# Kernel tuning notes

Measured on AMD Instinct MI355X. Metric: run time of the kernel, lower is better.

Reference implementation:

```python
import jax, jax.numpy as jnp
import numpy as np

B, S, H, V = 32, 512, 768, 30522
N_UPDATE, MAX_LEN = 3, 8
NEG_INF = -1e9


def setup_inputs() -> dict:
    key = jax.random.key(0)
    ks = jax.random.split(key, 12)
    x = jax.random.randint(ks[0], (B, S), 0, V, dtype=jnp.int32)
    decoder_input = jax.random.normal(ks[1], (B, N_UPDATE, H), dtype=jnp.float32)
    encoder_output = jax.random.normal(ks[2], (B, S, H), dtype=jnp.float32)
    hidden = jax.random.normal(ks[3], (1, B, H), dtype=jnp.float32)
    teacher = jax.random.randint(ks[4], (B, N_UPDATE, MAX_LEN), 0, V, dtype=jnp.int32)
    # tied embedding table, padding_idx=0 row zeroed
    embed_w = (jax.random.normal(ks[5], (V, H), dtype=jnp.float32) * 0.02).at[0].set(0.0)
    # GRU weights ~ N(0, initializer_range=0.02), biases zero (torch default biases exist; keep small random)
    gru_w_ih = jax.random.normal(ks[6], (3 * H, H), dtype=jnp.float32) * 0.02
    gru_w_hh = jax.random.normal(ks[7], (3 * H, H), dtype=jnp.float32) * 0.02
    gru_b_ih = jax.random.normal(ks[8], (3 * H,), dtype=jnp.float32) * 0.02
    gru_b_hh = jax.random.normal(ks[9], (3 * H,), dtype=jnp.float32) * 0.02
    wgen_w = jax.random.normal(ks[10], (1, 3 * H), dtype=jnp.float32) * 0.02
    wgen_b = jnp.zeros((1,), dtype=jnp.float32)
    return {"x": x, "decoder_input": decoder_input, "encoder_output": encoder_output,
            "hidden": hidden, "teacher": teacher, "embed_w": embed_w,
            "gru_w_ih": gru_w_ih, "gru_w_hh": gru_w_hh, "gru_b_ih": gru_b_ih,
            "gru_b_hh": gru_b_hh, "wgen_w": wgen_w, "wgen_b": wgen_b, "max_len": MAX_LEN}


def _gru_cell(w, h, w_ih, w_hh, b_ih, b_hh):
    # PyTorch GRU cell. w, h: [B, H]
    gi = w @ w_ih.T + b_ih  # [B, 3H]
    gh = h @ w_hh.T + b_hh
    i_r, i_z, i_n = jnp.split(gi, 3, axis=-1)
    h_r, h_z, h_n = jnp.split(gh, 3, axis=-1)
    r = jax.nn.sigmoid(i_r + h_r)
    z = jax.nn.sigmoid(i_z + h_z)
    n = jnp.tanh(i_n + r * h_n)
    return (1.0 - z) * n + z * h


def reference(x, decoder_input, encoder_output, hidden, teacher, embed_w,
              gru_w_ih, gru_w_hh, gru_b_ih, gru_b_hh, wgen_w, wgen_b, max_len):
    b, n_update, hid = decoder_input.shape
    vocab = embed_w.shape[0]
    mask = (x == 0)  # [B, S]
    bidx = jnp.arange(b)[:, None]

    # Teacher-forced inputs: step 0 of slot j uses decoder_input[:, j];
    # step k>0 uses embed(teacher[:, j, k-1]).
    teacher_emb = embed_w[teacher]                     # [B, nU, L, H]
    inputs = jnp.concatenate([decoder_input[:, :, None, :], teacher_emb[:, :, :-1, :]], axis=2)
    inputs = inputs.transpose(1, 2, 0, 3).reshape(n_update * max_len, b, hid)  # [nU*L, B, H]

    h0 = hidden[0]  # [B, H]

    def step(h, w):
        h = _gru_cell(w, h, gru_w_ih, gru_w_hh, gru_b_ih, gru_b_hh)
        attn_e = jnp.einsum('bsh,bh->bs', encoder_output, h)
        attn_e = jnp.where(mask, NEG_INF, attn_e)
        attn_history = jax.nn.softmax(attn_e, axis=-1)          # [B, S]
        attn_vocab = jax.nn.softmax(h @ embed_w.T, axis=-1)     # [B, V]
        context = jnp.einsum('bs,bsh->bh', attn_history, encoder_output)
        p_gen = jax.nn.sigmoid(jnp.concatenate([w, h, context], axis=-1) @ wgen_w.T + wgen_b)  # [B,1]
        p_ctx = jnp.zeros((b, vocab), dtype=attn_vocab.dtype).at[bidx, x].add(attn_history)
        p_final = p_gen * attn_vocab + (1.0 - p_gen) * p_ctx    # [B, V]
        return h, p_final

    _, p_all = jax.lax.scan(step, h0, inputs)                    # [nU*L, B, V]
    p_all = p_all.reshape(n_update, max_len, b, vocab).transpose(2, 0, 1, 3)
    return p_all  # [B, n_update, max_len, V]
```

## Files before the change

### kernel.cpp

```cpp
#include <hip/hip_runtime.h>
#include <cstdint>

#define B_  32
#define S_  512
#define H_  768
#define V_  30522
#define NT_ 24
#define H3  2304
#define NC4   (V_*H_/4)
#define NWALL (NT_*B_*H_)
#define NINIT (B_*H_)

#define GRU_NBLK 192
#define GRU_TPB  512
#define GRU_JPB  4
#define GRU_RPB  12

typedef unsigned short ushort_t;
typedef __attribute__((ext_vector_type(8))) short bf16x8;
typedef __attribute__((ext_vector_type(4))) float f32x4;

__device__ __forceinline__ ushort_t f2bf(float f){
  union { float f; unsigned u; } v; v.f = f;
  unsigned r = v.u + 0x7fffu + ((v.u >> 16) & 1u);
  return (ushort_t)(r >> 16);
}

__device__ __forceinline__ void load_lds_16B(const void* g, void* l){
  auto gp = reinterpret_cast<const __attribute__((address_space(1))) unsigned int*>(
      reinterpret_cast<uintptr_t>(g));
  auto lp = reinterpret_cast<__attribute__((address_space(3))) unsigned int*>(
      reinterpret_cast<uintptr_t>(l));
  __builtin_amdgcn_global_load_lds(gp, lp, 16, 0, 0);
}

__global__ void k_prep(const float* __restrict__ embed, const float* __restrict__ dec,
                       const int* __restrict__ teacher, const float* __restrict__ hidden,
                       ushort_t* __restrict__ E2, float* __restrict__ wall,
                       float* __restrict__ wallT, float* __restrict__ Hq, float* __restrict__ Hb,
                       float* __restrict__ pgacc, unsigned* __restrict__ flags){
  int idx = blockIdx.x * 256 + threadIdx.x;
  if (idx < NC4){
    float4 v = ((const float4*)embed)[idx];
    uint2 o;
    o.x = (unsigned)f2bf(v.x) | ((unsigned)f2bf(v.y) << 16);
    o.y = (unsigned)f2bf(v.z) | ((unsigned)f2bf(v.w) << 16);
    ((uint2*)E2)[idx] = o;
    return;
  }
  idx -= NC4;
  if (idx < NWALL){
    int k  = idx % H_;
    int rb = idx / H_;
    int t = rb >> 5, b = rb & 31;
    int jj = t >> 3, kk = t & 7;
    float v;
    if (kk == 0) v = dec[(b*3 + jj)*H_ + k];
    else { int tok = teacher[(b*3 + jj)*8 + kk - 1]; v = embed[(size_t)tok*H_ + k]; }
    wall[idx] = v;
    wallT[(size_t)t*24576 + ((k >> 1)*B_ + b)*2 + (k & 1)] = v;
    return;
  }
  idx -= NWALL;
  if (idx < NINIT){
    int b = idx / H_, k = idx % H_;
    float v = hidden[idx];
    Hb[idx] = v;
    Hq[((k >> 1)*B_ + b)*2 + (k & 1)] = v;
    return;
  }
  idx -= NINIT;
  if (idx < 768){ pgacc[idx] = 0.f; return; }
  idx -= 768;
  if (idx < 768) flags[idx] = 0u;
}

__global__ __launch_bounds__(GRU_TPB) void k_gru_all(const float* __restrict__ wallT, const float* __restrict__ wih,
                                                     const float* __restrict__ whh, const float* __restrict__ bih,
                                                     const float* __restrict__ bhh, const float* __restrict__ hidden,
                                                     float* __restrict__ Hq, float* __restrict__ Hb,
                                                     ushort_t* __restrict__ A2, unsigned* __restrict__ flags){
  __shared__ float wsh[GRU_RPB*768];
  __shared__ float wsi[GRU_RPB*768];
  __shared__ float red[16*776];
  __shared__ float bsh[GRU_RPB], bsi[GRU_RPB];
  const int tid = threadIdx.x;
  const int j0 = blockIdx.x * GRU_JPB;

  for (int idx4 = tid; idx4 < GRU_RPB*192; idx4 += GRU_TPB){
    int r = idx4 / 192, k4 = idx4 % 192;
    int gate = r >> 2, jl = r & 3;
    *(float4*)&wsh[r*768 + k4*4] = *(const float4*)&whh[(size_t)(gate*768 + j0 + jl)*768 + k4*4];
    *(float4*)&wsi[r*768 + k4*4] = *(const float4*)&wih[(size_t)(gate*768 + j0 + jl)*768 + k4*4];
  }
  if (tid < GRU_RPB){
    bsh[tid] = bhh[(tid >> 2)*768 + j0 + (tid & 3)];
    bsi[tid] = bih[(tid >> 2)*768 + j0 + (tid & 3)];
  }
  __syncthreads();

  const int ks = tid >> 5, b = tid & 31;
  const int jl = tid >> 5, bb = tid & 31;
  const int j  = j0 + (jl & 3);
  float hp = 0.f;
  if (tid < 128) hp = hidden[bb*768 + j];

  for (int t = 0; t < NT_; ++t){
    const unsigned long long* hsrc = (const unsigned long long*)(Hq + (size_t)t*24576);
    const float2* wsrc = (const float2*)(wallT + (size_t)t*24576);

    float acch[GRU_RPB], acci[GRU_RPB];
#pragma unroll
    for (int r = 0; r < GRU_RPB; ++r){ acch[r] = 0.f; acci[r] = 0.f; }
#pragma unroll 4
    for (int i = 0; i < 24; ++i){
      union { unsigned long long u; float f[2]; } cv;
      cv.u = __hip_atomic_load(&hsrc[(size_t)(ks*24 + i)*32 + b],
                               __ATOMIC_RELAXED, __HIP_MEMORY_SCOPE_AGENT);
      const float2 wv = wsrc[(size_t)(ks*24 + i)*32 + b];
      const float h0 = cv.f[0], h1 = cv.f[1];
#pragma unroll
      for (int r = 0; r < GRU_RPB; ++r){
        const float2 wh = *(const float2*)&wsh[r*768 + ks*48 + i*2];
        const float2 wi = *(const float2*)&wsi[r*768 + ks*48 + i*2];
        acch[r] += h0*wh.x + h1*wh.y;
        acci[r] += wv.x*wi.x + wv.y*wi.y;
      }
    }
#pragma unroll
    for (int r = 0; r < GRU_RPB; ++r){
      red[ks*776 + r*32 + b]             = acch[r];
      red[ks*776 + (GRU_RPB + r)*32 + b] = acci[r];
    }
    __syncthreads();

    if (tid < 128){
      float aR = 0.f, aZ = 0.f, aN = 0.f, iR = 0.f, iZ = 0.f, iN = 0.f;
#pragma unroll
      for (int k8 = 0; k8 < 16; ++k8){
        const float* rb_ = &red[k8*776 + jl*32 + bb];
        aR += rb_[0*128]; aZ += rb_[1*128]; aN += rb_[2*128];
        iR += rb_[3*128]; iZ += rb_[4*128]; iN += rb_[5*128];
      }
      aR += bsh[jl]; aZ += bsh[4 + jl]; aN += bsh[8 + jl];
      const float ir = iR + bsi[jl], iz = iZ + bsi[4 + jl], inn = iN + bsi[8 + jl];
      float rg = 1.f / (1.f + __expf(-(ir + aR)));
      float zg = 1.f / (1.f + __expf(-(iz + aZ)));
      float e2 = __expf(-2.f*(inn + rg * aN));
      float ng = (1.f - e2) / (1.f + e2);
      float hn = (1.f - zg)*ng + zg*hp;
      hp = hn;
      Hb[(size_t)(t+1)*24576 + bb*768 + j] = hn;
      A2[(size_t)(t*32 + bb)*768 + j] = f2bf(hn);
      if (t < NT_ - 1){
        union { float f; unsigned u; } hv; hv.f = hn;
        unsigned* hq32 = (unsigned*)(Hq + (size_t)(t+1)*24576);
        __hip_atomic_store(&hq32[((j >> 1)*32 + bb)*2 + (j & 1)], hv.u,
                           __ATOMIC_RELAXED, __HIP_MEMORY_SCOPE_AGENT);
      }
    }
    __syncthreads();

    if (t < NT_ - 1){
      if (tid == 0)
        __hip_atomic_store(&flags[(size_t)blockIdx.x*4], (unsigned)(t + 1),
                           __ATOMIC_RELAXED, __HIP_MEMORY_SCOPE_AGENT);
      if (tid < GRU_NBLK){
        unsigned spins = 0u;
        while (__hip_atomic_load(&flags[(size_t)tid*4], __ATOMIC_RELAXED,
                                 __HIP_MEMORY_SCOPE_AGENT) < (unsigned)(t + 1) &&
               ++spins < 20000000u)
          __builtin_amdgcn_s_sleep(1);
      }
      __syncthreads();
    }
  }
}

__global__ __launch_bounds__(256) void k_attn(const float* __restrict__ enc, const float* __restrict__ Hb1,
                                              float* __restrict__ ae){
  __shared__ float Es[64*36];
  __shared__ float Ht[24*36];
  const int b = blockIdx.x, s0 = blockIdx.y * 64;
  const int tid = threadIdx.x;
  const int s_l = tid & 63, tq = tid >> 6;
  const int r = tid >> 2, kq = tid & 3;
  float acc[6] = {0.f,0.f,0.f,0.f,0.f,0.f};
  for (int k0 = 0; k0 < 768; k0 += 32){
    __syncthreads();
    float4 e0 = *(const float4*)&enc[(size_t)(b*512 + s0 + r)*768 + k0 + kq*8];
    float4 e1 = *(const float4*)&enc[(size_t)(b*512 + s0 + r)*768 + k0 + kq*8 + 4];
    *(float4*)&Es[r*36 + kq*8]     = e0;
    *(float4*)&Es[r*36 + kq*8 + 4] = e1;
    if (tid < 192){
      int t = tid >> 3, k4 = tid & 7;
      *(float4*)&Ht[t*36 + k4*4] = *(const float4*)&Hb1[(size_t)t*24576 + b*768 + k0 + k4*4];
    }
    __syncthreads();
#pragma unroll
    for (int k4 = 0; k4 < 8; ++k4){
      float4 e = *(const float4*)&Es[s_l*36 + k4*4];
#pragma unroll
      for (int i = 0; i < 6; ++i){
        float4 h4 = *(const float4*)&Ht[(tq*6 + i)*36 + k4*4];
        acc[i] += e.x*h4.x + e.y*h4.y + e.z*h4.z + e.w*h4.w;
      }
    }
  }
#pragma unroll
  for (int i = 0; i < 6; ++i)
    ae[(size_t)((tq*6 + i)*32 + b)*512 + s0 + s_l] = acc[i];
}

__global__ __launch_bounds__(256) void k_attnsoft(const int* __restrict__ x, float* __restrict__ ae){
  const int row = blockIdx.x;
  const int b = row & 31;
  const int tid = threadIdx.x;
  __shared__ float red[256];
  float v0 = ae[(size_t)row*512 + tid];
  float v1 = ae[(size_t)row*512 + 256 + tid];
  if (x[b*512 + tid]        == 0) v0 = -1e9f;
  if (x[b*512 + 256 + tid]  == 0) v1 = -1e9f;
  float m = fmaxf(v0, v1);
  red[tid] = m; __syncthreads();
  for (int off = 128; off; off >>= 1){ if (tid < off) red[tid] = fmaxf(red[tid], red[tid+off]); __syncthreads(); }
  float M = red[0]; __syncthreads();
  float e0 = __expf(v0 - M), e1 = __expf(v1 - M);
  red[tid] = e0 + e1; __syncthreads();
  for (int off = 128; off; off >>= 1){ if (tid < off) red[tid] += red[tid+off]; __syncthreads(); }
  float inv = 1.f / red[0];
  ae[(size_t)row*512 + tid]       = e0 * inv;
  ae[(size_t)row*512 + 256 + tid] = e1 * inv;
}

__global__ __launch_bounds__(256) void k_ctx_pgen(const float* __restrict__ enc, const float* __restrict__ ah,
                                                  const float* __restrict__ wall, const float* __restrict__ Hb1,
                                                  const float* __restrict__ wg, float* __restrict__ pgacc){
  const int b = blockIdx.x;
  const int klane = threadIdx.x & 63;
  const int k = blockIdx.y * 64 + klane;
  const int tq = threadIdx.x >> 6;
  float acc[6] = {0.f,0.f,0.f,0.f,0.f,0.f};
  for (int s4 = 0; s4 < 512; s4 += 4){
    float e0 = enc[(size_t)(b*512 + s4 + 0)*768 + k];
    float e1 = enc[(size_t)(b*512 + s4 + 1)*768 + k];
    float e2 = enc[(size_t)(b*512 + s4 + 2)*768 + k];
    float e3 = enc[(size_t)(b*512 + s4 + 3)*768 + k];
#pragma unroll
    for (int i = 0; i < 6; ++i){
      float4 a4 = *(const float4*)&ah[(size_t)((tq*6 + i)*32 + b)*512 + s4];
      acc[i] = fmaf(a4.x, e0, acc[i]); acc[i] = fmaf(a4.y, e1, acc[i]);
      acc[i] = fmaf(a4.z, e2, acc[i]); acc[i] = fmaf(a4.w, e3, acc[i]);
    }
  }
  const float wgk = wg[k], wgh = wg[768 + k], wgc = wg[1536 + k];
#pragma unroll
  for (int i = 0; i < 6; ++i){
    const int t = tq*6 + i, row = t*32 + b;
    float p = acc[i]*wgc + wall[(size_t)row*768 + k]*wgk + Hb1[(size_t)t*24576 + b*768 + k]*wgh;
#pragma unroll
    for (int off = 32; off; off >>= 1) p += __shfl_down(p, off, 64);
    if (klane == 0) atomicAdd(&pgacc[row], p);
  }
}

__global__ __launch_bounds__(256) void k_vgemm(const ushort_t* __restrict__ A2, const ushort_t* __restrict__ E2,
                                               float* __restrict__ out){
  __shared__ ushort_t ldsA[128*64];
  __shared__ ushort_t ldsB[128*64];
  const int wg = blockIdx.x;
  const int xcd = wg & 7, qq = wg >> 3;
  const int ntile = (qq / 6) * 8 + xcd;
  const int mtile = qq % 6;
  const int tid = threadIdx.x;
  const int w = tid >> 6, lane = tid & 63;
  const int lrow = lane >> 3, lpos = lane & 7;
  const int wm = w >> 1, wn = w & 1;
  const int q = lane >> 4, fr = lane & 15;
  f32x4 acc[4][4];
  f32x4 zero = {0.f, 0.f, 0.f, 0.f};
#pragma unroll
  for (int a = 0; a < 4; ++a)
#pragma unroll
    for (int c = 0; c < 4; ++c) acc[a][c] = zero;

  for (int k0 = 0; k0 < 768; k0 += 64){
    __syncthreads();
#pragma unroll
    for (int i = 0; i < 4; ++i){
      int row = w*32 + i*8 + lrow;
      int c   = lpos ^ (row & 7);
      const ushort_t* srcA = A2 + (size_t)(mtile*128 + row)*768 + k0 + c*8;
      int brow = ntile*128 + row; if (brow > V_ - 1) brow = V_ - 1;
      const ushort_t* srcB = E2 + (size_t)brow*768 + k0 + c*8;
      load_lds_16B(srcA, &ldsA[row*64 + lpos*8]);
      load_lds_16B(srcB, &ldsB[row*64 + lpos*8]);
    }
    __builtin_amdgcn_s_waitcnt(0);
    __syncthreads();
#pragma unroll
    for (int s = 0; s < 2; ++s){
      bf16x8 af[4], bfr[4];
#pragma unroll
      for (int mt = 0; mt < 4; ++mt){
        int row = wm*64 + mt*16 + fr;
        int ch = (s*4 + q) ^ (row & 7);
        af[mt] = *(const bf16x8*)&ldsA[row*64 + ch*8];
      }
#pragma unroll
      for (int nt = 0; nt < 4; ++nt){
        int row = wn*64 + nt*16 + fr;
        int ch = (s*4 + q) ^ (row & 7);
        bfr[nt] = *(const bf16x8*)&ldsB[row*64 + ch*8];
      }
#pragma unroll
      for (int mt = 0; mt < 4; ++mt)
#pragma unroll
        for (int nt = 0; nt < 4; ++nt)
          acc[mt][nt] = __builtin_amdgcn_mfma_f32_16x16x32_bf16(af[mt], bfr[nt], acc[mt][nt], 0, 0, 0);
    }
  }
#pragma unroll
  for (int mt = 0; mt < 4; ++mt){
#pragma unroll
    for (int nt = 0; nt < 4; ++nt){
      int gn = ntile*128 + wn*64 + nt*16 + fr;
      if (gn >= V_) continue;
#pragma unroll
      for (int rg = 0; rg < 4; ++rg){
        int gm = mtile*128 + wm*64 + mt*16 + q*4 + rg;
        int t = gm >> 5, b = gm & 31;
        out[(size_t)(b*24 + t)*V_ + gn] = acc[mt][nt][rg];
      }
    }
  }
}

__global__ __launch_bounds__(512) void k_vsoft(float* __restrict__ out, const float* __restrict__ pgacc,
                                               const float* __restrict__ wgb){
  const int row = blockIdx.x;
  const int b = row / 24, t = row % 24;
  const float pg = 1.f / (1.f + __expf(-(pgacc[t*32 + b] + wgb[0])));
  const int tid = threadIdx.x;
  float* rp = out + (size_t)row * V_;
  const float4* rp4 = (const float4*)rp;
  float m = -3.0e38f, s = 0.f;
  for (int i = tid; i < 7630; i += 512){
    float4 v = rp4[i];
    float vm = fmaxf(fmaxf(v.x, v.y), fmaxf(v.z, v.w));
    float vs = __expf(v.x - vm) + __expf(v.y - vm) + __expf(v.z - vm) + __expf(v.w - vm);
    float nm = fmaxf(m, vm);
    s = s * __expf(m - nm) + vs * __expf(vm - nm);
    m = nm;
  }
  if (tid < 2){
    float v = rp[30520 + tid];
    float nm = fmaxf(m, v);
    s = s * __expf(m - nm) + __expf(v - nm);
    m = nm;
  }
#pragma unroll
  for (int off = 1; off < 64; off <<= 1){
    float m2 = __shfl_xor(m, off, 64), s2 = __shfl_xor(s, off, 64);
    float nm = fmaxf(m, m2);
    s = s*__expf(m - nm) + s2*__expf(m2 - nm);
    m = nm;
  }
  __shared__ float rm[8], rs[8];
  const int wid = tid >> 6;
  if ((tid & 63) == 0){ rm[wid] = m; rs[wid] = s; }
  __syncthreads();
  if (tid == 0){
    float M = rm[0], S = rs[0];
#pragma unroll
    for (int i = 1; i < 8; ++i){
      float m2 = rm[i], s2 = rs[i];
      float nm = fmaxf(M, m2);
      S = S*__expf(M - nm) + s2*__expf(m2 - nm);
      M = nm;
    }
    rm[0] = M; rs[0] = pg / S;
  }
  __syncthreads();
  const float M = rm[0], inv = rs[0];
  for (int i = tid; i < 7630; i += 512){
    float4 v = rp4[i];
    v.x = __expf(v.x - M) * inv;
    v.y = __expf(v.y - M) * inv;
    v.z = __expf(v.z - M) * inv;
    v.w = __expf(v.w - M) * inv;
    ((float4*)rp)[i] = v;
  }
  if (tid < 2) rp[30520 + tid] = __expf(rp[30520 + tid] - M) * inv;
}

__global__ void k_scatter(const float* __restrict__ ah, const float* __restrict__ pgacc,
                          const float* __restrict__ wgb, const int* __restrict__ x,
                          float* __restrict__ out){
  int idx = blockIdx.x * 256 + threadIdx.x;
  int s = idx & 511;
  int row = idx >> 9;
  int t = row >> 5, b = row & 31;
  float pg = 1.f / (1.f + __expf(-(pgacc[row] + wgb[0])));
  float val = ah[idx] * (1.f - pg);
  int col = x[b*512 + s];
  atomicAdd(&out[(size_t)(b*24 + t)*V_ + col], val);
}

extern "C" void kernel_launch(void* const* d_in, const int* in_sizes, int n_in,
                              void* d_out, int out_size, void* d_ws, size_t ws_size,
                              hipStream_t stream){
  (void)in_sizes; (void)n_in; (void)out_size; (void)ws_size;
  const int*   x      = (const int*)  d_in[0];
  const float* dec    = (const float*)d_in[1];
  const float* enc    = (const float*)d_in[2];
  const float* hidden = (const float*)d_in[3];
  const int*   teach  = (const int*)  d_in[4];
  const float* embed  = (const float*)d_in[5];
  const float* wih    = (const float*)d_in[6];
  const float* whh    = (const float*)d_in[7];
  const float* bih    = (const float*)d_in[8];
  const float* bhh    = (const float*)d_in[9];
  const float* wg     = (const float*)d_in[10];
  const float* wgb    = (const float*)d_in[11];
  float* out = (float*)d_out;

  char* p = (char*)d_ws;
  auto alloc = [&](size_t bytes){ void* r = (void*)p; p += (bytes + 255) & ~(size_t)255; return r; };
  ushort_t* E2  = (ushort_t*)alloc((size_t)V_ * H_ * 2);
  ushort_t* A2  = (ushort_t*)alloc((size_t)768 * 768 * 2);
  float* wall   = (float*)alloc((size_t)NT_ * B_ * H_ * 4);
  float* wallT  = (float*)alloc((size_t)NT_ * B_ * H_ * 4);
  float* Hb     = (float*)alloc((size_t)(NT_+1) * B_ * H_ * 4);
  float* Hq     = (float*)alloc((size_t)(NT_+1) * B_ * H_ * 4);
  float* ae     = (float*)alloc((size_t)NT_ * B_ * S_ * 4);
  float* pgacc  = (float*)alloc(768 * 4);
  unsigned* flags = (unsigned*)alloc(768 * 4);

  const int prep_items  = NC4 + NWALL + NINIT + 768 + 768;
  const int prep_blocks = (prep_items + 255) / 256;

  k_prep<<<prep_blocks, 256, 0, stream>>>(embed, dec, teach, hidden, E2, wall, wallT, Hq, Hb, pgacc, flags);
  k_gru_all<<<GRU_NBLK, GRU_TPB, 0, stream>>>(wallT, wih, whh, bih, bhh, hidden, Hq, Hb, A2, flags);
  k_attn<<<dim3(32, 8), 256, 0, stream>>>(enc, Hb + 24576, ae);
  k_attnsoft<<<768, 256, 0, stream>>>(x, ae);
  k_ctx_pgen<<<dim3(32, 12), 256, 0, stream>>>(enc, ae, wall, Hb + 24576, wg, pgacc);
  k_vgemm<<<1440, 256, 0, stream>>>(A2, E2, out);
  k_vsoft<<<768, 512, 0, stream>>>(out, pgacc, wgb);
  k_scatter<<<(NT_*B_*S_)/256, 256, 0, stream>>>(ae, pgacc, wgb, x, out);
}
```

Before: 706.4 us.

## Fuse softmax partial stats into vocab GEMM epilogue and scatter into softmax

The vocab GEMM epilogue now computes per-tile online max/sum-exp for each output row and writes them to a small stats buffer. The softmax kernel merges these tile stats instead of re-reading each 30522-wide row for the max/sum pass. The scatter-add of attention is folded into the end of the softmax kernel, with block-local atomics removing one launch. The GRU inner loop is also reworked to batch its global loads into registers and use float4 LDS reads, at the cost of more registers.

```diff
diff --git a/kernel.cpp b/kernel.cpp
--- a/kernel.cpp
+++ b/kernel.cpp
@@ -15,6 +15,7 @@
 #define GRU_TPB  512
 #define GRU_JPB  4
 #define GRU_RPB  12
+#define NTILE_   240
 
 typedef unsigned short ushort_t;
 typedef __attribute__((ext_vector_type(8))) short bf16x8;
@@ -112,19 +113,33 @@
     float acch[GRU_RPB], acci[GRU_RPB];
 #pragma unroll
     for (int r = 0; r < GRU_RPB; ++r){ acch[r] = 0.f; acci[r] = 0.f; }
-#pragma unroll 4
-    for (int i = 0; i < 24; ++i){
-      union { unsigned long long u; float f[2]; } cv;
-      cv.u = __hip_atomic_load(&hsrc[(size_t)(ks*24 + i)*32 + b],
-                               __ATOMIC_RELAXED, __HIP_MEMORY_SCOPE_AGENT);
-      const float2 wv = wsrc[(size_t)(ks*24 + i)*32 + b];
-      const float h0 = cv.f[0], h1 = cv.f[1];
-#pragma unroll
-      for (int r = 0; r < GRU_RPB; ++r){
-        const float2 wh = *(const float2*)&wsh[r*768 + ks*48 + i*2];
-        const float2 wi = *(const float2*)&wsi[r*768 + ks*48 + i*2];
-        acch[r] += h0*wh.x + h1*wh.y;
-        acci[r] += wv.x*wi.x + wv.y*wi.y;
+
+#pragma unroll
+    for (int c = 0; c < 2; ++c){
+      unsigned long long hreg[12];
+      float2 wreg[12];
+#pragma unroll
+      for (int i = 0; i < 12; ++i)
+        hreg[i] = __hip_atomic_load(&hsrc[(size_t)(ks*24 + c*12 + i)*32 + b],
+                                    __ATOMIC_RELAXED, __HIP_MEMORY_SCOPE_AGENT);
+#pragma unroll
+      for (int i = 0; i < 12; ++i)
+        wreg[i] = wsrc[(size_t)(ks*24 + c*12 + i)*32 + b];
+
+#pragma unroll
+      for (int p = 0; p < 6; ++p){
+        union { unsigned long long u; float f[2]; } ca, cb;
+        ca.u = hreg[2*p]; cb.u = hreg[2*p + 1];
+        const float h0a = ca.f[0], h1a = ca.f[1], h0b = cb.f[0], h1b = cb.f[1];
+        const float2 wa = wreg[2*p], wb = wreg[2*p + 1];
+        const int wo = ks*48 + c*24 + p*4;
+#pragma unroll
+        for (int r = 0; r < GRU_RPB; ++r){
+          const float4 wh = *(const float4*)&wsh[r*768 + wo];
+          const float4 wi = *(const float4*)&wsi[r*768 + wo];
+          acch[r] += h0a*wh.x + h1a*wh.y + h0b*wh.z + h1b*wh.w;
+          acci[r] += wa.x*wi.x + wa.y*wi.y + wb.x*wi.z + wb.y*wi.w;
+        }
       }
     }
 #pragma unroll
@@ -265,9 +280,10 @@
 }
 
 __global__ __launch_bounds__(256) void k_vgemm(const ushort_t* __restrict__ A2, const ushort_t* __restrict__ E2,
-                                               float* __restrict__ out){
+                                               float* __restrict__ out, float2* __restrict__ vstat){
   __shared__ ushort_t ldsA[128*64];
   __shared__ ushort_t ldsB[128*64];
+  __shared__ float smx[128*2], sms[128*2];
   const int wg = blockIdx.x;
   const int xcd = wg & 7, qq = wg >> 3;
   const int ntile = (qq / 6) * 8 + xcd;
@@ -323,41 +339,57 @@
 #pragma unroll
   for (int mt = 0; mt < 4; ++mt){
 #pragma unroll
-    for (int nt = 0; nt < 4; ++nt){
-      int gn = ntile*128 + wn*64 + nt*16 + fr;
-      if (gn >= V_) continue;
-#pragma unroll
-      for (int rg = 0; rg < 4; ++rg){
-        int gm = mtile*128 + wm*64 + mt*16 + q*4 + rg;
-        int t = gm >> 5, b = gm & 31;
-        out[(size_t)(b*24 + t)*V_ + gn] = acc[mt][nt][rg];
-      }
-    }
-  }
-}
-
-__global__ __launch_bounds__(512) void k_vsoft(float* __restrict__ out, const float* __restrict__ pgacc,
-                                               const float* __restrict__ wgb){
+    for (int rg = 0; rg < 4; ++rg){
+      float m = -3.0e38f, ssum = 0.f;
+#pragma unroll
+      for (int nt = 0; nt < 4; ++nt){
+        int gn = ntile*128 + wn*64 + nt*16 + fr;
+        if (gn < V_){
+          float v = acc[mt][nt][rg];
+          int gm = mtile*128 + wm*64 + mt*16 + q*4 + rg;
+          int t = gm >> 5, b = gm & 31;
+          out[(size_t)(b*24 + t)*V_ + gn] = v;
+          float nm = fmaxf(m, v);
+          ssum = ssum*__expf(m - nm) + __expf(v - nm);
+          m = nm;
+        }
+      }
+#pragma unroll
+      for (int off = 1; off < 16; off <<= 1){
+        float m2 = __shfl_xor(m, off, 64), s2 = __shfl_xor(ssum, off, 64);
+        float nm = fmaxf(m, m2);
+        ssum = ssum*__expf(m - nm) + s2*__expf(m2 - nm);
+        m = nm;
+      }
+      if (fr == 0){
+        int rl = wm*64 + mt*16 + q*4 + rg;
+        smx[rl*2 + wn] = m; sms[rl*2 + wn] = ssum;
+      }
+    }
+  }
+  __syncthreads();
+  if (tid < 128){
+    float m0 = smx[tid*2], s0 = sms[tid*2], m1 = smx[tid*2 + 1], s1 = sms[tid*2 + 1];
+    float nm = fmaxf(m0, m1);
+    float ss = s0*__expf(m0 - nm) + s1*__expf(m1 - nm);
+    int gm = mtile*128 + tid;
+    int t = gm >> 5, b2 = gm & 31;
+    vstat[(size_t)(b2*24 + t)*NTILE_ + ntile] = make_float2(nm, ss);
+  }
+}
+
+__global__ __launch_bounds__(512) void k_vsoft_sc(float* __restrict__ out, const float* __restrict__ pgacc,
+                                                  const float* __restrict__ wgb, const float2* __restrict__ vstat,
+                                                  const float* __restrict__ ah, const int* __restrict__ x){
   const int row = blockIdx.x;
   const int b = row / 24, t = row % 24;
   const float pg = 1.f / (1.f + __expf(-(pgacc[t*32 + b] + wgb[0])));
   const int tid = threadIdx.x;
   float* rp = out + (size_t)row * V_;
-  const float4* rp4 = (const float4*)rp;
   float m = -3.0e38f, s = 0.f;
-  for (int i = tid; i < 7630; i += 512){
-    float4 v = rp4[i];
-    float vm = fmaxf(fmaxf(v.x, v.y), fmaxf(v.z, v.w));
-    float vs = __expf(v.x - vm) + __expf(v.y - vm) + __expf(v.z - vm) + __expf(v.w - vm);
-    float nm = fmaxf(m, vm);
-    s = s * __expf(m - nm) + vs * __expf(vm - nm);
-    m = nm;
-  }
-  if (tid < 2){
-    float v = rp[30520 + tid];
-    float nm = fmaxf(m, v);
-    s = s * __expf(m - nm) + __expf(v - nm);
-    m = nm;
+  if (tid < NTILE_){
+    float2 st = vstat[(size_t)row*NTILE_ + tid];
+    m = st.x; s = st.y;
   }
 #pragma unroll
   for (int off = 1; off < 64; off <<= 1){
@@ -383,6 +415,7 @@
   }
   __syncthreads();
   const float M = rm[0], inv = rs[0];
+  const float4* rp4 = (const float4*)rp;
   for (int i = tid; i < 7630; i += 512){
     float4 v = rp4[i];
     v.x = __expf(v.x - M) * inv;
@@ -392,19 +425,12 @@
     ((float4*)rp)[i] = v;
   }
   if (tid < 2) rp[30520 + tid] = __expf(rp[30520 + tid] - M) * inv;
-}
-
-__global__ void k_scatter(const float* __restrict__ ah, const float* __restrict__ pgacc,
-                          const float* __restrict__ wgb, const int* __restrict__ x,
-                          float* __restrict__ out){
-  int idx = blockIdx.x * 256 + threadIdx.x;
-  int s = idx & 511;
-  int row = idx >> 9;
-  int t = row >> 5, b = row & 31;
-  float pg = 1.f / (1.f + __expf(-(pgacc[row] + wgb[0])));
-  float val = ah[idx] * (1.f - pg);
-  int col = x[b*512 + s];
-  atomicAdd(&out[(size_t)(b*24 + t)*V_ + col], val);
+  __syncthreads();
+  {
+    float val = ah[(size_t)(t*32 + b)*512 + tid] * (1.f - pg);
+    int col = x[b*512 + tid];
+    __hip_atomic_fetch_add(&rp[col], val, __ATOMIC_RELAXED, __HIP_MEMORY_SCOPE_WORKGROUP);
+  }
 }
 
 extern "C" void kernel_launch(void* const* d_in, const int* in_sizes, int n_in,
@@ -434,6 +460,7 @@
   float* Hb     = (float*)alloc((size_t)(NT_+1) * B_ * H_ * 4);
   float* Hq     = (float*)alloc((size_t)(NT_+1) * B_ * H_ * 4);
   float* ae     = (float*)alloc((size_t)NT_ * B_ * S_ * 4);
+  float2* vstat = (float2*)alloc((size_t)768 * NTILE_ * 8);
   float* pgacc  = (float*)alloc(768 * 4);
   unsigned* flags = (unsigned*)alloc(768 * 4);
 
@@ -445,7 +472,6 @@
   k_attn<<<dim3(32, 8), 256, 0, stream>>>(enc, Hb + 24576, ae);
   k_attnsoft<<<768, 256, 0, stream>>>(x, ae);
   k_ctx_pgen<<<dim3(32, 12), 256, 0, stream>>>(enc, ae, wall, Hb + 24576, wg, pgacc);
-  k_vgemm<<<1440, 256, 0, stream>>>(A2, E2, out);
-  k_vsoft<<<768, 512, 0, stream>>>(out, pgacc, wgb);
-  k_scatter<<<(NT_*B_*S_)/256, 256, 0, stream>>>(ae, pgacc, wgb, x, out);
-}
+  k_vgemm<<<1440, 256, 0, stream>>>(A2, E2, out, vstat);
+  k_vsoft_sc<<<768, 512, 0, stream>>>(out, pgacc, wgb, vstat, ae, x);
+}
```

Result: faster. 670.8 us (-5.0%).
